# Optimization experiments

Hardware: AMD Instinct MI355X
Metric: run time of the kernel (lower is better)

## Reference

```python
import jax, jax.numpy as jnp
import numpy as np

T, B, DIM, N = 2048, 16, 1024, 64
INIT_BETA_BIAS = 2.0
EPS = 1e-6


def setup_inputs() -> dict:
    key = jax.random.key(0)
    ks = jax.random.split(key, 6)
    xavier = np.sqrt(2.0 / (N + DIM)).astype(np.float32)
    return {
        "x": jax.random.normal(ks[0], (T, B, DIM), dtype=jnp.float32),
        "S0": jnp.zeros((B, N, N), dtype=jnp.float32),
        "W_k": jax.random.normal(ks[1], (N, DIM), dtype=jnp.float32) * xavier,
        "W_v": jax.random.normal(ks[2], (N, DIM), dtype=jnp.float32) * xavier,
        "W_q": jax.random.normal(ks[3], (N, DIM), dtype=jnp.float32) * xavier,
        "W_beta": jax.random.normal(ks[4], (N, DIM), dtype=jnp.float32) * xavier,
        "b_beta": jnp.full((N,), INIT_BETA_BIAS, dtype=jnp.float32),
    }


def reference(x, S0, W_k, W_v, W_q, W_beta, b_beta):
    # Batched projections: [T, B, dim] @ [dim, n] -> [T, B, n]
    k_all = jnp.einsum("tbd,nd->tbn", x, W_k)
    v_all = jnp.einsum("tbd,nd->tbn", x, W_v)
    q_all = jnp.einsum("tbd,nd->tbn", x, W_q)
    g_all = jax.nn.sigmoid(jnp.einsum("tbd,nd->tbn", x, W_beta) + b_beta)

    def step(S, inp):
        k, v, q, g = inp  # each [B, n]
        k_norm = k / (jnp.linalg.norm(k, axis=-1, keepdims=True) + EPS)
        retrieved = jnp.einsum("bij,bj->bi", S, k_norm)
        delta = v - retrieved
        S_new = g[:, :, None] * S + delta[:, :, None] * k_norm[:, None, :]
        Sq = jnp.einsum("bij,bj->bi", S_new, q)
        out = Sq * jax.nn.silu(Sq)  # self-gated output
        return S_new, out

    S_final, output = jax.lax.scan(step, S0, (k_all, v_all, q_all, g_all))
    return output, S_final
```

## Files before the change

### kernel.cpp

```cpp
#include <hip/hip_runtime.h>
#include <math.h>

#define T_STEPS 2048
#define BATCH   16
#define DIM     1024
#define NSTATE  64
#define NFIELD  256
#define PROJ_TSTRIDE (BATCH * NFIELD)
static constexpr float EPS = 1e-6f;

#define AS1 __attribute__((address_space(1)))
#define AS3 __attribute__((address_space(3)))

typedef _Float16 f16x8 __attribute__((ext_vector_type(8)));
typedef float    f32x4 __attribute__((ext_vector_type(4)));


__device__ __forceinline__ f16x8 cvt8(const float4 a, const float4 b) {
    f16x8 r;
    r[0] = (_Float16)a.x; r[1] = (_Float16)a.y;
    r[2] = (_Float16)a.z; r[3] = (_Float16)a.w;
    r[4] = (_Float16)b.x; r[5] = (_Float16)b.y;
    r[6] = (_Float16)b.z; r[7] = (_Float16)b.w;
    return r;
}

#define PBM   128
#define KSTEP 64
#define NKS   (DIM / KSTEP)

__global__ __launch_bounds__(512, 2) void proj_mfma(
    const float* __restrict__ x,
    const float* __restrict__ Wk, const float* __restrict__ Wv,
    const float* __restrict__ Wq, const float* __restrict__ Wb,
    const float* __restrict__ bb,
    float* __restrict__ proj)
{
    __shared__ _Float16 Asub[2][16][64][8];
    __shared__ _Float16 Bsub[2][32][64][8];

    const int tid = threadIdx.x;
    const int w   = tid >> 6, wl = tid & 63;
    const int wm  = w >> 2,  wn = w & 3;
    const int l15 = wl & 15, lr = wl >> 4;
    const size_t mbase = (size_t)blockIdx.x * PBM;

    const float* apA[2];
    #pragma unroll
    for (int j = 0; j < 2; ++j) {
        const int st = w + 8 * j, rg = st & 7, kc = st >> 3;
        apA[j] = x + (mbase + rg * 16 + l15) * DIM + kc * 32 + lr * 8;
    }
    const float* apB[4];
    #pragma unroll
    for (int j = 0; j < 4; ++j) {
        const int st = w + 8 * j, cg = st & 15, kcb = st >> 4;
        const int col = cg * 16 + l15, field = cg >> 2, wrow = col & 63;
        const float* Wf = (field == 0 ? Wk : field == 1 ? Wv : field == 2 ? Wq : Wb);
        apB[j] = Wf + (size_t)wrow * DIM + kcb * 32 + lr * 8;
    }

    float4 hA[2][2], hB[4][2];
    auto load_regs = [&](int ks) {
        const int k0 = ks * KSTEP;
        #pragma unroll
        for (int j = 0; j < 2; ++j) {
            hA[j][0] = *(const float4*)(apA[j] + k0);
            hA[j][1] = *(const float4*)(apA[j] + k0 + 4);
        }
        #pragma unroll
        for (int j = 0; j < 4; ++j) {
            hB[j][0] = *(const float4*)(apB[j] + k0);
            hB[j][1] = *(const float4*)(apB[j] + k0 + 4);
        }
    };
    auto write_lds = [&](int buf) {
        #pragma unroll
        for (int j = 0; j < 2; ++j)
            *(f16x8*)&Asub[buf][w + 8 * j][wl][0] = cvt8(hA[j][0], hA[j][1]);
        #pragma unroll
        for (int j = 0; j < 4; ++j)
            *(f16x8*)&Bsub[buf][w + 8 * j][wl][0] = cvt8(hB[j][0], hB[j][1]);
    };

    f32x4 acc[4][4] = {};

    load_regs(0);
    write_lds(0);
    __syncthreads();

    for (int ks = 0; ks < NKS; ++ks) {
        const int buf = ks & 1;
        if (ks + 1 < NKS) load_regs(ks + 1);

        #pragma unroll
        for (int kc = 0; kc < 2; ++kc) {
            f16x8 af[4], bf[4];
            #pragma unroll
            for (int mf = 0; mf < 4; ++mf)
                af[mf] = *(const f16x8*)&Asub[buf][kc * 8 + wm * 4 + mf][wl][0];
            #pragma unroll
            for (int nf = 0; nf < 4; ++nf)
                bf[nf] = *(const f16x8*)&Bsub[buf][kc * 16 + wn * 4 + nf][wl][0];
            #pragma unroll
            for (int mf = 0; mf < 4; ++mf)
                #pragma unroll
                for (int nf = 0; nf < 4; ++nf)
                    acc[mf][nf] = __builtin_amdgcn_mfma_f32_16x16x32_f16(
                        af[mf], bf[nf], acc[mf][nf], 0, 0, 0);
        }

        if (ks + 1 < NKS) write_lds(buf ^ 1);
        __syncthreads();
    }

    if (wn == 0) {
        #pragma unroll
        for (int mf = 0; mf < 4; ++mf) {
            f32x4 s = acc[mf][0] * acc[mf][0];
            #pragma unroll
            for (int nf = 1; nf < 4; ++nf) s += acc[mf][nf] * acc[mf][nf];
            #pragma unroll
            for (int r = 0; r < 4; ++r) {
                float t = s[r];
                t += __shfl_xor(t, 1); t += __shfl_xor(t, 2);
                t += __shfl_xor(t, 4); t += __shfl_xor(t, 8);
                const float sc = 1.f / (sqrtf(t) + EPS);
                #pragma unroll
                for (int nf = 0; nf < 4; ++nf) acc[mf][nf][r] *= sc;
            }
        }
    }
    if (wn == 3) {
        #pragma unroll
        for (int nf = 0; nf < 4; ++nf) {
            const float bv = bb[nf * 16 + l15];
            #pragma unroll
            for (int mf = 0; mf < 4; ++mf)
                #pragma unroll
                for (int r = 0; r < 4; ++r)
                    acc[mf][nf][r] = 1.f / (1.f + __expf(-(acc[mf][nf][r] + bv)));
        }
    }

    #pragma unroll
    for (int mf = 0; mf < 4; ++mf)
        #pragma unroll
        for (int r = 0; r < 4; ++r) {
            float* dst = proj + (mbase + wm * 64 + mf * 16 + lr * 4 + r) * NFIELD
                              + wn * 64 + l15;
            dst[0]  = acc[mf][0][r];
            dst[16] = acc[mf][1][r];
            dst[32] = acc[mf][2][r];
            dst[48] = acc[mf][3][r];
        }
}


template <int CTRL>
__device__ __forceinline__ float dpp_add(float x) {
    int yi = __builtin_amdgcn_update_dpp(0, __float_as_int(x), CTRL, 0xF, 0xF, true);
    return x + __int_as_float(yi);
}
__device__ __forceinline__ float reduce16(float x) {
    x = dpp_add<0x121>(x);
    x = dpp_add<0x122>(x);
    x = dpp_add<0x124>(x);
    x = dpp_add<0x128>(x);
    return x;
}
__device__ __forceinline__ float dot4r(const float4& u, const float4& w) {
    float t0 = u.x * w.x; t0 = fmaf(u.y, w.y, t0);
    float t1 = u.z * w.z; t1 = fmaf(u.w, w.w, t1);
    return reduce16(t0 + t1);
}

#define CH 32
#define NCHUNK (T_STEPS / CH)

__global__ __launch_bounds__(128) void scan_kernel(
    const float* __restrict__ proj,
    const float* __restrict__ S0,
    float* __restrict__ out,
    float* __restrict__ Sfin)
{
    __shared__ float KQ[2][CH][128];
    __shared__ float VG[2][CH][16];

    const int tid = threadIdx.x;
    const int l   = tid & 15;
    const int grp = tid >> 4;
    const int b   = blockIdx.x >> 3;
    const int i0  = (blockIdx.x & 7) * 8;
    const int i   = i0 + grp;
    const int c0  = l * 4;

    const size_t srow = ((size_t)(b * 64 + i)) * 64 + c0;
    float4 S = *(const float4*)(S0 + srow);

    const float* pb = proj + (size_t)b * NFIELD;
    const int wid = tid >> 6, wl = tid & 63;

    const int l31  = wl & 31;
    const int kq_f = l31 * 4 + ((l31 >= 16) ? 64 : 0);
    const int kq_s = wl >> 5;
    const int idx  = wl & 15;
    const int vg_f = (idx & 1) ? (192 + i0 + (idx >> 1)) : (64 + i0 + (idx >> 1));
    const int vg_s = wl >> 4;

    auto stage = [&](int c, int nb) {
        const float* cbase = pb + (size_t)c * CH * PROJ_TSTRIDE;
        #pragma unroll
        for (int m = 0; m < 8; ++m) {
            const int n = wid * 8 + m;
            const float* g = cbase + (size_t)(2 * n + kq_s) * PROJ_TSTRIDE + kq_f;
            void* lp = (char*)&KQ[nb][0][0] + n * 1024;
            __builtin_amdgcn_global_load_lds((const AS1 void*)g, (AS3 void*)lp, 16, 0, 0);
        }
        #pragma unroll
        for (int m = 0; m < 4; ++m) {
            const int p = wid * 4 + m;
            const float* g = cbase + (size_t)(4 * p + vg_s) * PROJ_TSTRIDE + vg_f;
            void* lp = (char*)&VG[nb][0][0] + p * 256;
            __builtin_amdgcn_global_load_lds((const AS1 void*)g, (AS3 void*)lp, 4, 0, 0);
        }
    };

    float4 kn_s[4], q_s[4];
    float2 vg_s4[4];
    auto ldslot = [&](int cb, int s, int j) {
        kn_s[j]  = *(const float4*)(&KQ[cb][s][c0]);
        q_s[j]   = *(const float4*)(&KQ[cb][s][64 + c0]);
        vg_s4[j] = *(const float2*)(&VG[cb][s][2 * grp]);
    };

    stage(0, 0);
    __syncthreads();

    float a;
    auto prime = [&](int nb) {
        #pragma unroll
        for (int j = 0; j < 4; ++j) ldslot(nb, j, j);
        a = dot4r(S, kn_s[0]);
    };
    prime(0);

    float osel = 0.f;

    for (int c = 0; c < NCHUNK; ++c) {
        const int cb = c & 1;
        const bool more = (c + 1 < NCHUNK);
        if (more) stage(c + 1, cb ^ 1);

        #pragma unroll
        for (int s = 0; s < CH; ++s) {
            const int j = s & 3;
            const float4 kn = kn_s[j], q = q_s[j];
            const float  v = vg_s4[j].x, g = vg_s4[j].y;

            if (s + 4 < CH) ldslot(cb, s + 4, j);

            const float d = v - a;
            S.x = fmaf(d, kn.x, g * S.x);
            S.y = fmaf(d, kn.y, g * S.y);
            S.z = fmaf(d, kn.z, g * S.z);
            S.w = fmaf(d, kn.w, g * S.w);

            const float sq = dot4r(S, q);
            if (s + 1 < CH) a = dot4r(S, kn_s[(s + 1) & 3]);

            osel = ((s & 15) == l) ? sq : osel;
            if ((s & 15) == 15) {
                const int tbase = c * CH + (s - 15);
                out[((size_t)(tbase + l) * BATCH + b) * 64 + i] = osel;
            }
        }

        if (more) {
            __syncthreads();
            prime(cb ^ 1);
        }
    }

    *(float4*)(Sfin + srow) = S;
}

__global__ __launch_bounds__(256) void silu_kernel(float* __restrict__ out) {
    const int idx = blockIdx.x * 256 + threadIdx.x;
    float4* p = (float4*)out + idx;
    float4 x = *p;
    x.x = x.x * x.x / (1.f + __expf(-x.x));
    x.y = x.y * x.y / (1.f + __expf(-x.y));
    x.z = x.z * x.z / (1.f + __expf(-x.z));
    x.w = x.w * x.w / (1.f + __expf(-x.w));
    *p = x;
}

extern "C" void kernel_launch(void* const* d_in, const int* in_sizes, int n_in,
                              void* d_out, int out_size, void* d_ws, size_t ws_size,
                              hipStream_t stream) {
    const float* x  = (const float*)d_in[0];
    const float* S0 = (const float*)d_in[1];
    const float* Wk = (const float*)d_in[2];
    const float* Wv = (const float*)d_in[3];
    const float* Wq = (const float*)d_in[4];
    const float* Wb = (const float*)d_in[5];
    const float* bb = (const float*)d_in[6];

    float* out  = (float*)d_out;
    float* Sfin = out + (size_t)T_STEPS * BATCH * NSTATE;
    float* proj = (float*)d_ws;

    proj_mfma<<<(T_STEPS * BATCH) / PBM, 512, 0, stream>>>(x, Wk, Wv, Wq, Wb, bb, proj);
    scan_kernel<<<(BATCH * NSTATE) / 8, 128, 0, stream>>>(proj, S0, out, Sfin);
    silu_kernel<<<(T_STEPS * BATCH * NSTATE) / 4 / 256, 256, 0, stream>>>(out);
}
```

Measured before the change: 442.1 us.

## Shorten scan critical path via precomputed key overlaps, fp16 weight prep, fused silu

The serial scan's next retrieval S_new·k_{t+1} is rewritten as g*(S·k_{t+1}) + d*(k_t·k_{t+1}). The S·k_{t+1} part can be computed before the state update, and the key overlap comes from a new kappa kernel and is staged into LDS. This takes one dot-product reduction off the per-step dependency chain. Weights are converted to fp16 once in a prep kernel and loaded with direct global-to-LDS loads in the projection GEMM, and the A tile load layout is reorganised. The silu kernel is folded into the scan's output store. In exchange there are two extra launches and a slightly different rounding order for the retrieval.

```diff
diff --git a/kernel.cpp b/kernel.cpp
--- a/kernel.cpp
+++ b/kernel.cpp
@@ -13,85 +13,127 @@
 #define AS3 __attribute__((address_space(3)))
 
 typedef _Float16 f16x8 __attribute__((ext_vector_type(8)));
+typedef _Float16 f16x4 __attribute__((ext_vector_type(4)));
 typedef float    f32x4 __attribute__((ext_vector_type(4)));
 
-
-__device__ __forceinline__ f16x8 cvt8(const float4 a, const float4 b) {
-    f16x8 r;
-    r[0] = (_Float16)a.x; r[1] = (_Float16)a.y;
-    r[2] = (_Float16)a.z; r[3] = (_Float16)a.w;
-    r[4] = (_Float16)b.x; r[5] = (_Float16)b.y;
-    r[6] = (_Float16)b.z; r[7] = (_Float16)b.w;
-    return r;
-}
+template <int CTRL>
+__device__ __forceinline__ float dpp_add(float x) {
+    int yi = __builtin_amdgcn_update_dpp(0, __float_as_int(x), CTRL, 0xF, 0xF, true);
+    return x + __int_as_float(yi);
+}
+__device__ __forceinline__ float reduce16(float x) {
+    x = dpp_add<0x121>(x);
+    x = dpp_add<0x122>(x);
+    x = dpp_add<0x124>(x);
+    x = dpp_add<0x128>(x);
+    return x;
+}
+__device__ __forceinline__ float dot4r(const float4& u, const float4& w) {
+    float t0 = u.x * w.x; t0 = fmaf(u.y, w.y, t0);
+    float t1 = u.z * w.z; t1 = fmaf(u.w, w.w, t1);
+    return reduce16(t0 + t1);
+}
+
 
 #define PBM   128
 #define KSTEP 64
 #define NKS   (DIM / KSTEP)
 
-__global__ __launch_bounds__(512, 2) void proj_mfma(
-    const float* __restrict__ x,
+__global__ __launch_bounds__(256) void prep_w16(
     const float* __restrict__ Wk, const float* __restrict__ Wv,
     const float* __restrict__ Wq, const float* __restrict__ Wb,
-    const float* __restrict__ bb,
-    float* __restrict__ proj)
+    _Float16* __restrict__ W16)
+{
+    const int flat = blockIdx.x * 256 + threadIdx.x;
+    const int lane = flat & 63;
+    const int st   = (flat >> 6) & 31;
+    const int ks   = flat >> 11;
+    const int cg = st & 15, kc2 = st >> 4;
+    const int col = cg * 16 + (lane & 15);
+    const int field = col >> 6, wrow = col & 63;
+    const float* Wf = (field == 0 ? Wk : field == 1 ? Wv : field == 2 ? Wq : Wb);
+    const float* src = Wf + (size_t)wrow * DIM + ks * 64 + kc2 * 32 + (lane >> 4) * 8;
+    const float4 a = *(const float4*)(src);
+    const float4 b = *(const float4*)(src + 4);
+    f16x8 r;
+    r[0] = (_Float16)a.x; r[1] = (_Float16)a.y; r[2] = (_Float16)a.z; r[3] = (_Float16)a.w;
+    r[4] = (_Float16)b.x; r[5] = (_Float16)b.y; r[6] = (_Float16)b.z; r[7] = (_Float16)b.w;
+    *(f16x8*)(W16 + (size_t)flat * 8) = r;
+}
+
+__global__ __launch_bounds__(512, 2) void proj_mfma(
+    const float* __restrict__ x, const _Float16* __restrict__ W16,
+    const float* __restrict__ bb, float* __restrict__ proj)
 {
     __shared__ _Float16 Asub[2][16][64][8];
     __shared__ _Float16 Bsub[2][32][64][8];
 
     const int tid = threadIdx.x;
-    const int w   = tid >> 6, wl = tid & 63;
-    const int wm  = w >> 2,  wn = w & 3;
+    const int w = tid >> 6, wl = tid & 63;
+    const int wm = w >> 2, wn = w & 3;
     const int l15 = wl & 15, lr = wl >> 4;
     const size_t mbase = (size_t)blockIdx.x * PBM;
 
-    const float* apA[2];
+    _Float16* const abase = &Asub[0][0][0][0];
+    _Float16* const bbase = &Bsub[0][0][0][0];
+
+    const float* asrc[4];
+    int aoff[4];
     #pragma unroll
-    for (int j = 0; j < 2; ++j) {
-        const int st = w + 8 * j, rg = st & 7, kc = st >> 3;
-        apA[j] = x + (mbase + rg * 16 + l15) * DIM + kc * 32 + lr * 8;
-    }
-    const float* apB[4];
+    for (int it = 0; it < 4; ++it) {
+        const int fid = it * 512 + tid;
+        const int row = fid >> 4, kq = (fid & 15) * 4;
+        asrc[it] = x + (mbase + row) * (size_t)DIM + kq;
+        aoff[it] = ((kq >> 5) * 8 + (row >> 4)) * 512
+                 + ((row & 15) + ((kq >> 3) & 3) * 16) * 8
+                 + (kq & 7);
+    }
+    const _Float16* bsrc[4];
+    int boff[4];
     #pragma unroll
-    for (int j = 0; j < 4; ++j) {
-        const int st = w + 8 * j, cg = st & 15, kcb = st >> 4;
-        const int col = cg * 16 + l15, field = cg >> 2, wrow = col & 63;
-        const float* Wf = (field == 0 ? Wk : field == 1 ? Wv : field == 2 ? Wq : Wb);
-        apB[j] = Wf + (size_t)wrow * DIM + kcb * 32 + lr * 8;
-    }
-
-    float4 hA[2][2], hB[4][2];
-    auto load_regs = [&](int ks) {
-        const int k0 = ks * KSTEP;
-        #pragma unroll
-        for (int j = 0; j < 2; ++j) {
-            hA[j][0] = *(const float4*)(apA[j] + k0);
-            hA[j][1] = *(const float4*)(apA[j] + k0 + 4);
-        }
-        #pragma unroll
-        for (int j = 0; j < 4; ++j) {
-            hB[j][0] = *(const float4*)(apB[j] + k0);
-            hB[j][1] = *(const float4*)(apB[j] + k0 + 4);
-        }
-    };
-    auto write_lds = [&](int buf) {
-        #pragma unroll
-        for (int j = 0; j < 2; ++j)
-            *(f16x8*)&Asub[buf][w + 8 * j][wl][0] = cvt8(hA[j][0], hA[j][1]);
-        #pragma unroll
-        for (int j = 0; j < 4; ++j)
-            *(f16x8*)&Bsub[buf][w + 8 * j][wl][0] = cvt8(hB[j][0], hB[j][1]);
+    for (int m = 0; m < 4; ++m) {
+        const int st = w * 4 + m;
+        bsrc[m] = W16 + ((size_t)st * 64 + wl) * 8;
+        boff[m] = st * 512;
+    }
+
+    auto stageB = [&](int ks, int buf) {
+        #pragma unroll
+        for (int m = 0; m < 4; ++m) {
+            const _Float16* g = bsrc[m] + (size_t)ks * 16384;
+            void* lp = (char*)bbase + (size_t)(buf * 16384 + boff[m]) * 2;
+            __builtin_amdgcn_global_load_lds((const AS1 void*)g, (AS3 void*)lp, 16, 0, 0);
+        }
+    };
+
+    float4 ha[4];
+    auto loadA = [&](int ks) {
+        #pragma unroll
+        for (int it = 0; it < 4; ++it)
+            ha[it] = *(const float4*)(asrc[it] + ks * KSTEP);
+    };
+    auto writeA = [&](int buf) {
+        #pragma unroll
+        for (int it = 0; it < 4; ++it) {
+            f16x4 h;
+            h[0] = (_Float16)ha[it].x; h[1] = (_Float16)ha[it].y;
+            h[2] = (_Float16)ha[it].z; h[3] = (_Float16)ha[it].w;
+            *(f16x4*)(abase + buf * 8192 + aoff[it]) = h;
+        }
     };
 
     f32x4 acc[4][4] = {};
 
-    load_regs(0);
-    write_lds(0);
+    stageB(0, 0);
+    loadA(0); writeA(0);
     __syncthreads();
 
     for (int ks = 0; ks < NKS; ++ks) {
         const int buf = ks & 1;
-        if (ks + 1 < NKS) load_regs(ks + 1);
+        if (ks + 1 < NKS) {
+            stageB(ks + 1, buf ^ 1);
+            loadA(ks + 1);
+        }
 
         #pragma unroll
         for (int kc = 0; kc < 2; ++kc) {
@@ -110,7 +152,7 @@
                         af[mf], bf[nf], acc[mf][nf], 0, 0, 0);
         }
 
-        if (ks + 1 < NKS) write_lds(buf ^ 1);
+        if (ks + 1 < NKS) writeA(buf ^ 1);
         __syncthreads();
     }
 
@@ -156,36 +198,39 @@
         }
 }
 
-
-template <int CTRL>
-__device__ __forceinline__ float dpp_add(float x) {
-    int yi = __builtin_amdgcn_update_dpp(0, __float_as_int(x), CTRL, 0xF, 0xF, true);
-    return x + __int_as_float(yi);
-}
-__device__ __forceinline__ float reduce16(float x) {
-    x = dpp_add<0x121>(x);
-    x = dpp_add<0x122>(x);
-    x = dpp_add<0x124>(x);
-    x = dpp_add<0x128>(x);
-    return x;
-}
-__device__ __forceinline__ float dot4r(const float4& u, const float4& w) {
-    float t0 = u.x * w.x; t0 = fmaf(u.y, w.y, t0);
-    float t1 = u.z * w.z; t1 = fmaf(u.w, w.w, t1);
-    return reduce16(t0 + t1);
-}
+#define KAP_T 2112
+
+__global__ __launch_bounds__(256) void kappa_kernel(
+    const float* __restrict__ proj, float* __restrict__ kap)
+{
+    const int tid = threadIdx.x;
+    const int gid = blockIdx.x * 16 + (tid >> 4);
+    const int l   = tid & 15;
+    const int t = gid >> 4, b = gid & 15;
+    if (t == 0 || t >= T_STEPS) {
+        if (l == 0) kap[gid] = 0.f;
+        return;
+    }
+    const float4 u = *(const float4*)(proj + ((size_t)t * BATCH + b) * NFIELD + 4 * l);
+    const float4 w = *(const float4*)(proj + ((size_t)(t - 1) * BATCH + b) * NFIELD + 4 * l);
+    const float p = dot4r(u, w);
+    if (l == 0) kap[gid] = p;
+}
+
 
 #define CH 32
 #define NCHUNK (T_STEPS / CH)
 
 __global__ __launch_bounds__(128) void scan_kernel(
     const float* __restrict__ proj,
+    const float* __restrict__ kap,
     const float* __restrict__ S0,
     float* __restrict__ out,
     float* __restrict__ Sfin)
 {
     __shared__ float KQ[2][CH][128];
     __shared__ float VG[2][CH][16];
+    __shared__ float KP[2][64];
 
     const int tid = threadIdx.x;
     const int l   = tid & 15;
@@ -224,6 +269,11 @@
             void* lp = (char*)&VG[nb][0][0] + p * 256;
             __builtin_amdgcn_global_load_lds((const AS1 void*)g, (AS3 void*)lp, 4, 0, 0);
         }
+        if (wid == 0) {
+            const float* g = kap + ((size_t)(c * CH + wl + 1) * BATCH + b);
+            void* lp = (char*)&KP[nb][0];
+            __builtin_amdgcn_global_load_lds((const AS1 void*)g, (AS3 void*)lp, 4, 0, 0);
+        }
     };
 
     float4 kn_s[4], q_s[4];
@@ -258,6 +308,13 @@
             const float4 kn = kn_s[j], q = q_s[j];
             const float  v = vg_s4[j].x, g = vg_s4[j].y;
 
+            float cpart = 0.f, kap_n = 0.f;
+            if (s + 1 < CH) {
+                const float4 knn = kn_s[(s + 1) & 3];
+                kap_n = KP[cb][s];
+                cpart = dot4r(S, knn);
+            }
+
             if (s + 4 < CH) ldslot(cb, s + 4, j);
 
             const float d = v - a;
@@ -267,12 +324,13 @@
             S.w = fmaf(d, kn.w, g * S.w);
 
             const float sq = dot4r(S, q);
-            if (s + 1 < CH) a = dot4r(S, kn_s[(s + 1) & 3]);
+            if (s + 1 < CH) a = fmaf(d, kap_n, g * cpart);
 
             osel = ((s & 15) == l) ? sq : osel;
             if ((s & 15) == 15) {
+                const float y = osel * osel / (1.f + __expf(-osel));
                 const int tbase = c * CH + (s - 15);
-                out[((size_t)(tbase + l) * BATCH + b) * 64 + i] = osel;
+                out[((size_t)(tbase + l) * BATCH + b) * 64 + i] = y;
             }
         }
 
@@ -283,17 +341,6 @@
     }
 
     *(float4*)(Sfin + srow) = S;
-}
-
-__global__ __launch_bounds__(256) void silu_kernel(float* __restrict__ out) {
-    const int idx = blockIdx.x * 256 + threadIdx.x;
-    float4* p = (float4*)out + idx;
-    float4 x = *p;
-    x.x = x.x * x.x / (1.f + __expf(-x.x));
-    x.y = x.y * x.y / (1.f + __expf(-x.y));
-    x.z = x.z * x.z / (1.f + __expf(-x.z));
-    x.w = x.w * x.w / (1.f + __expf(-x.w));
-    *p = x;
 }
 
 extern "C" void kernel_launch(void* const* d_in, const int* in_sizes, int n_in,
@@ -309,9 +356,13 @@
 
     float* out  = (float*)d_out;
     float* Sfin = out + (size_t)T_STEPS * BATCH * NSTATE;
-    float* proj = (float*)d_ws;
-
-    proj_mfma<<<(T_STEPS * BATCH) / PBM, 512, 0, stream>>>(x, Wk, Wv, Wq, Wb, bb, proj);
-    scan_kernel<<<(BATCH * NSTATE) / 8, 128, 0, stream>>>(proj, S0, out, Sfin);
-    silu_kernel<<<(T_STEPS * BATCH * NSTATE) / 4 / 256, 256, 0, stream>>>(out);
-}
+
+    float*    proj = (float*)d_ws;
+    float*    kap  = proj + (size_t)T_STEPS * BATCH * NFIELD;
+    _Float16* W16  = (_Float16*)(kap + (size_t)KAP_T * BATCH);
+
+    prep_w16<<<128, 256, 0, stream>>>(Wk, Wv, Wq, Wb, W16);
+    proj_mfma<<<(T_STEPS * BATCH) / PBM, 512, 0, stream>>>(x, W16, bb, proj);
+    kappa_kernel<<<KAP_T, 256, 0, stream>>>(proj, kap);
+    scan_kernel<<<(BATCH * NSTATE) / 8, 128, 0, stream>>>(proj, kap, S0, out, Sfin);
+}
```

After: 424.8 us. 1.04x faster.
